# Kernel optimization log

Measured on AMD Instinct MI355X. Metric: run time of the kernel, lower is better.

Reference implementation:

```python
import jax, jax.numpy as jnp
import numpy as np

INPUT_SIZE = 300
HIDDEN = 128
NUM_CLASSES = 2
B, T = 256, 512


def setup_inputs() -> dict:
    key = jax.random.key(0)
    ks = jax.random.split(key, 7)
    s_ih = 1.0 / np.sqrt(HIDDEN)
    x = jax.random.normal(ks[0], (B, T, INPUT_SIZE), dtype=jnp.float32)
    W_ih = jax.random.uniform(ks[1], (HIDDEN, INPUT_SIZE), minval=-s_ih, maxval=s_ih, dtype=jnp.float32)
    W_hh = jax.random.uniform(ks[2], (HIDDEN, HIDDEN), minval=-s_ih, maxval=s_ih, dtype=jnp.float32)
    b_ih = jax.random.uniform(ks[3], (HIDDEN,), minval=-s_ih, maxval=s_ih, dtype=jnp.float32)
    b_hh = jax.random.uniform(ks[4], (HIDDEN,), minval=-s_ih, maxval=s_ih, dtype=jnp.float32)
    fc_w = jax.random.uniform(ks[5], (NUM_CLASSES, HIDDEN), minval=-s_ih, maxval=s_ih, dtype=jnp.float32)
    fc_b = jax.random.uniform(ks[6], (NUM_CLASSES,), minval=-s_ih, maxval=s_ih, dtype=jnp.float32)
    return {"x": x, "W_ih": W_ih, "W_hh": W_hh, "b_ih": b_ih, "b_hh": b_hh, "fc_w": fc_w, "fc_b": fc_b}


def reference(x, W_ih, W_hh, b_ih, b_hh, fc_w, fc_b):
    # Precompute input projections for all timesteps: [B,T,H]
    xp = jnp.einsum('bti,hi->bth', x, W_ih) + b_ih + b_hh
    h0 = jnp.zeros((x.shape[0], HIDDEN), dtype=x.dtype)

    def step(h, xp_t):  # xp_t: [B,H]
        h_new = jnp.tanh(xp_t + h @ W_hh.T)
        return h_new, None

    h_last, _ = jax.lax.scan(step, h0, jnp.swapaxes(xp, 0, 1))  # scan over T
    # Final FC on last hidden state (out[:, -1, :] of the RNN outputs)
    return h_last @ fc_w.T + fc_b
```

## Files before the change

kernel.cpp:

```cpp
#include <hip/hip_runtime.h>
#include <cstdint>
#include <cstddef>

#define KIN 300
#define KPAD 320
#define HIDDEN 128
#define BSZ 256
#define TSZ 512

#define ASTR 332
#define ST1 2176
#define HSTR 136

typedef __attribute__((ext_vector_type(8))) short short8;
typedef __attribute__((ext_vector_type(4))) short s16x4;
typedef __attribute__((ext_vector_type(4))) float f32x4;

__device__ __forceinline__ short f2bf(float f) {
  uint32_t u = __builtin_bit_cast(uint32_t, f);
  u = (u + 0x7FFFu + ((u >> 16) & 1u)) >> 16;
  return (short)u;
}
__device__ __forceinline__ float bf2f(short s) {
  uint32_t u = ((uint32_t)(uint16_t)s) << 16;
  return __builtin_bit_cast(float, u);
}
__device__ __forceinline__ float bflo(uint32_t u) {
  return __builtin_bit_cast(float, u << 16);
}
__device__ __forceinline__ float bfhi(uint32_t u) {
  return __builtin_bit_cast(float, u & 0xFFFF0000u);
}
__device__ __forceinline__ uint32_t pack2bf(float a, float b) {
  uint32_t r;
  asm("v_cvt_pk_bf16_f32 %0, %1, %2" : "=v"(r) : "v"(a), "v"(b));
  return r;
}
__device__ __forceinline__ float tanhf_fast(float v) {
  const float e = __builtin_amdgcn_exp2f(v * 2.88539008177793f);
  return fmaf(-2.0f, __builtin_amdgcn_rcpf(e + 1.0f), 1.0f);
}
__device__ __forceinline__ void barrier_lds() {
  asm volatile("s_waitcnt lgkmcnt(0)\n\ts_barrier" ::: "memory");
}
__device__ __forceinline__ void barrier_all() {
  asm volatile("s_waitcnt vmcnt(0) lgkmcnt(0)\n\ts_barrier" ::: "memory");
}
__device__ __forceinline__ void dma16(const short* g, short* l) {
  __builtin_amdgcn_global_load_lds(
      (const __attribute__((address_space(1))) void*)g,
      (__attribute__((address_space(3))) void*)l, 16, 0, 0);
}

__global__ __launch_bounds__(256) void wcvt_bf16(const float* __restrict__ W,
                                                 short* __restrict__ W16) {
  const int i = blockIdx.x * 256 + threadIdx.x;
  if (i >= HIDDEN * KPAD) return;
  const int n = i / KPAD, k = i % KPAD;
  W16[i] = (k < KIN) ? f2bf(W[n * KIN + k]) : (short)0;
}

__global__ __launch_bounds__(256) void xp_gemm_mfma(
    const float* __restrict__ x, const short* __restrict__ W16,
    const float* __restrict__ b_ih, const float* __restrict__ b_hh,
    short* __restrict__ xp16) {
  __shared__ __align__(16) short As[64 * ASTR];
  const int tid = threadIdx.x;
  const int lane = tid & 63, w = tid >> 6;
  const int q = lane >> 4, c = lane & 15;
  const int bg = blockIdx.x & 15, tc = blockIdx.x >> 4;
  const int b0 = bg * 16, t0 = tc * 4;

#pragma unroll
  for (int i = 0; i < 19; ++i) {
    const int f = tid + 256 * i;
    if (f < 4800) {
      const int rr = f / 75;
      const int k4 = f - rr * 75;
      const int b_in = rr >> 2, t_loc = rr & 3;
      const float4 v = *(const float4*)(
          x + ((size_t)(b0 + b_in) * TSZ + t0 + t_loc) * KIN + k4 * 4);
      uint2 pv;
      pv.x = pack2bf(v.x, v.y);
      pv.y = pack2bf(v.z, v.w);
      *(uint2*)&As[rr * ASTR + k4 * 4] = pv;
    }
  }
  if (tid < 64) {
    const uint2 z = {0u, 0u};
#pragma unroll
    for (int j = 0; j < 5; ++j) *(uint2*)&As[tid * ASTR + 300 + j * 4] = z;
  }
  __syncthreads();

  f32x4 acc[2][4];
#pragma unroll
  for (int ht = 0; ht < 2; ++ht)
#pragma unroll
    for (int rt = 0; rt < 4; ++rt) acc[ht][rt] = (f32x4){0.f, 0.f, 0.f, 0.f};

  const short* wp0 = W16 + (size_t)((2 * w + 0) * 16 + c) * KPAD + q * 8;
  const short* wp1 = W16 + (size_t)((2 * w + 1) * 16 + c) * KPAD + q * 8;
  const short* bqp = &As[c * ASTR + q * 8];
  short8 af[2][2];
  short8 bq[2][4];
  af[0][0] = *(const short8*)(wp0);
  af[0][1] = *(const short8*)(wp1);
#pragma unroll
  for (int rt = 0; rt < 4; ++rt)
    bq[0][rt] = *(const short8*)(bqp + rt * 16 * ASTR);
#pragma unroll
  for (int kc = 0; kc < 10; ++kc) {
    const int cur = kc & 1;
    if (kc < 9) {
      af[cur ^ 1][0] = *(const short8*)(wp0 + (kc + 1) * 32);
      af[cur ^ 1][1] = *(const short8*)(wp1 + (kc + 1) * 32);
#pragma unroll
      for (int rt = 0; rt < 4; ++rt)
        bq[cur ^ 1][rt] = *(const short8*)(bqp + rt * 16 * ASTR + (kc + 1) * 32);
    }
#pragma unroll
    for (int ht = 0; ht < 2; ++ht)
#pragma unroll
      for (int rt = 0; rt < 4; ++rt)
        acc[ht][rt] = __builtin_amdgcn_mfma_f32_16x16x32_bf16(
            af[cur][ht], bq[cur][rt], acc[ht][rt], 0, 0, 0);
  }
  __syncthreads();

  float4 bsum[2];
#pragma unroll
  for (int ht = 0; ht < 2; ++ht) {
    const int h0 = (2 * w + ht) * 16 + q * 4;
    const float4 bi = *(const float4*)(b_ih + h0);
    const float4 bh = *(const float4*)(b_hh + h0);
    bsum[ht] = make_float4(bi.x + bh.x, bi.y + bh.y, bi.z + bh.z, bi.w + bh.w);
  }
#pragma unroll
  for (int ht = 0; ht < 2; ++ht) {
    const int g = (2 * w + ht) * 4 + q;
    const int u = 4 * (g >> 3) + (g & 3);
    const int mt = (g >> 2) & 1;
#pragma unroll
    for (int rt = 0; rt < 4; ++rt) {
      const int b_in = rt * 4 + (c >> 2);
      const int t_loc = c & 3;
      uint2 pv;
      pv.x = pack2bf(acc[ht][rt][0] + bsum[ht].x, acc[ht][rt][1] + bsum[ht].y);
      pv.y = pack2bf(acc[ht][rt][2] + bsum[ht].z, acc[ht][rt][3] + bsum[ht].w);
      *(uint2*)&As[t_loc * ST1 + u * 136 + b_in * 8 + mt * 4] = pv;
    }
  }
  __syncthreads();
#pragma unroll
  for (int i = 0; i < 4; ++i) {
    const int4 vv =
        *(const int4*)&As[i * ST1 + (tid >> 4) * 136 + (tid & 15) * 8];
    *(int4*)(xp16 + ((size_t)(t0 + i) * 16 + bg) * 2048 + tid * 8) = vv;
  }
}

__global__ __launch_bounds__(256, 1) void rnn_scan_dma(
    const short* __restrict__ xp16, const float* __restrict__ Whh,
    const float* __restrict__ fc_w, const float* __restrict__ fc_b,
    float* __restrict__ out) {
  __shared__ __align__(16) short xs[2][8][2048];
  __shared__ __align__(16) short ht[2][16][HSTR];
  const int tid = threadIdx.x;
  const int lane = tid & 63, w = tid >> 6;
  const int q = lane >> 4, c = lane & 15;
  const int bg = blockIdx.x;

  short8 aw[2][4];
#pragma unroll
  for (int mt = 0; mt < 2; ++mt)
#pragma unroll
    for (int kc = 0; kc < 4; ++kc) {
      const float* src =
          Whh + (size_t)(32 * w + 16 * mt + c) * HIDDEN + kc * 32 + q * 8;
      const float4 v0 = *(const float4*)(src);
      const float4 v1 = *(const float4*)(src + 4);
      short8 t;
      t[0] = f2bf(v0.x); t[1] = f2bf(v0.y); t[2] = f2bf(v0.z); t[3] = f2bf(v0.w);
      t[4] = f2bf(v1.x); t[5] = f2bf(v1.y); t[6] = f2bf(v1.z); t[7] = f2bf(v1.w);
      aw[mt][kc] = t;
    }

  {
    uint32_t* z = (uint32_t*)&ht[0][0][0];
    for (int i = tid; i < 2176; i += 256) z[i] = 0;
  }

#define ISSUE_CHUNK(CH, BUF)                                                  \
  {                                                                           \
    _Pragma("unroll") for (int sr = 0; sr < 2; ++sr) {                        \
      const int s = 2 * w + sr;                                               \
      const short* srcb =                                                     \
          xp16 + ((size_t)((CH)*8 + s) * 16 + bg) * 2048 + lane * 8;          \
      _Pragma("unroll") for (int j = 0; j < 4; ++j)                           \
          dma16(srcb + j * 512, &xs[BUF][s][j * 512]);                        \
    }                                                                         \
  }

  ISSUE_CHUNK(0, 0)
  barrier_all();

  const int xsoff = (4 * w + q) * 128 + c * 8;
  const f32x4 zero4 = {0.f, 0.f, 0.f, 0.f};

  for (int cc = 0; cc < 64; ++cc) {
    const int buf = cc & 1;
    if (cc + 1 < 64) ISSUE_CHUNK(cc + 1, buf ^ 1)
    uint4 us[8];
#pragma unroll
    for (int s = 0; s < 8; ++s) us[s] = *(const uint4*)&xs[buf][s][xsoff];
#pragma unroll
    for (int s = 0; s < 8; ++s) {
      const int rb = s & 1;
      const short* bp = &ht[rb][c][q * 8];
      const short8 bh0 = *(const short8*)(bp + 0);
      const short8 bh1 = *(const short8*)(bp + 32);
      const short8 bh2 = *(const short8*)(bp + 64);
      const short8 bh3 = *(const short8*)(bp + 96);
      f32x4 p0 = {bflo(us[s].x), bfhi(us[s].x), bflo(us[s].y), bfhi(us[s].y)};
      f32x4 p1 = {bflo(us[s].z), bfhi(us[s].z), bflo(us[s].w), bfhi(us[s].w)};
      f32x4 r0 = zero4, r1 = zero4;
      p0 = __builtin_amdgcn_mfma_f32_16x16x32_bf16(aw[0][0], bh0, p0, 0, 0, 0);
      r0 = __builtin_amdgcn_mfma_f32_16x16x32_bf16(aw[0][2], bh2, r0, 0, 0, 0);
      p1 = __builtin_amdgcn_mfma_f32_16x16x32_bf16(aw[1][0], bh0, p1, 0, 0, 0);
      r1 = __builtin_amdgcn_mfma_f32_16x16x32_bf16(aw[1][2], bh2, r1, 0, 0, 0);
      p0 = __builtin_amdgcn_mfma_f32_16x16x32_bf16(aw[0][1], bh1, p0, 0, 0, 0);
      r0 = __builtin_amdgcn_mfma_f32_16x16x32_bf16(aw[0][3], bh3, r0, 0, 0, 0);
      p1 = __builtin_amdgcn_mfma_f32_16x16x32_bf16(aw[1][1], bh1, p1, 0, 0, 0);
      r1 = __builtin_amdgcn_mfma_f32_16x16x32_bf16(aw[1][3], bh3, r1, 0, 0, 0);
      const f32x4 s0 = p0 + r0;
      const f32x4 s1 = p1 + r1;
      uint2 w0, w1;
      w0.x = pack2bf(tanhf_fast(s0[0]), tanhf_fast(s0[1]));
      w0.y = pack2bf(tanhf_fast(s0[2]), tanhf_fast(s0[3]));
      w1.x = pack2bf(tanhf_fast(s1[0]), tanhf_fast(s1[1]));
      w1.y = pack2bf(tanhf_fast(s1[2]), tanhf_fast(s1[3]));
      *(uint2*)&ht[rb ^ 1][c][32 * w + 4 * q] = w0;
      *(uint2*)&ht[rb ^ 1][c][32 * w + 16 + 4 * q] = w1;
      barrier_lds();
    }
    barrier_all();
  }
#undef ISSUE_CHUNK

  if (tid < 32) {
    const int bi = tid >> 1, cls = tid & 1;
    float s = fc_b[cls];
    const float* fw = fc_w + cls * HIDDEN;
#pragma unroll 8
    for (int k = 0; k < HIDDEN; k += 4) {
      s = fmaf(bf2f(ht[0][bi][k + 0]), fw[k + 0], s);
      s = fmaf(bf2f(ht[0][bi][k + 1]), fw[k + 1], s);
      s = fmaf(bf2f(ht[0][bi][k + 2]), fw[k + 2], s);
      s = fmaf(bf2f(ht[0][bi][k + 3]), fw[k + 3], s);
    }
    out[(bg * 16 + bi) * 2 + cls] = s;
  }
}

extern "C" void kernel_launch(void* const* d_in, const int* in_sizes, int n_in,
                              void* d_out, int out_size, void* d_ws, size_t ws_size,
                              hipStream_t stream) {
  const float* x    = (const float*)d_in[0];
  const float* W_ih = (const float*)d_in[1];
  const float* W_hh = (const float*)d_in[2];
  const float* b_ih = (const float*)d_in[3];
  const float* b_hh = (const float*)d_in[4];
  const float* fc_w = (const float*)d_in[5];
  const float* fc_b = (const float*)d_in[6];
  short* xp16 = (short*)d_ws;
  short* W16  = (short*)((char*)d_ws + (33u << 20));
  float* out  = (float*)d_out;

  wcvt_bf16<<<(HIDDEN * KPAD + 255) / 256, 256, 0, stream>>>(W_ih, W16);
  xp_gemm_mfma<<<16 * (TSZ / 4), 256, 0, stream>>>(x, W16, b_ih, b_hh, xp16);
  rnn_scan_dma<<<16, 256, 0, stream>>>(xp16, W_hh, fc_w, fc_b, out);
}
```

Measured before the change: 455.5 us.

## Run two independent batch recurrences per 512-thread block with swizzled hidden state

The scan kernel now uses 8 blocks of 512 threads, each running two independent 16-row batch recurrences (one per group of four waves) that share the block barriers, instead of 16 blocks of 256 threads. Hidden-state LDS storage moves to an XOR-swizzled layout without padding, meant to avoid bank conflicts. Chunks now hold 4 timesteps over 128 iterations rather than 8 over 64. The aim is to interleave two recurrence chains on one CU to hide MFMA and tanh latency, but it uses half as many CUs and each barrier now waits on both chains and more waves.

```diff
diff --git a/kernel.cpp b/kernel.cpp
--- a/kernel.cpp
+++ b/kernel.cpp
@@ -10,7 +10,6 @@
 
 #define ASTR 332
 #define ST1 2176
-#define HSTR 136
 
 typedef __attribute__((ext_vector_type(8))) short short8;
 typedef __attribute__((ext_vector_type(4))) short s16x4;
@@ -160,16 +159,18 @@
   }
 }
 
-__global__ __launch_bounds__(256, 1) void rnn_scan_dma(
+__global__ __launch_bounds__(512, 1) void rnn_scan_dma(
     const short* __restrict__ xp16, const float* __restrict__ Whh,
     const float* __restrict__ fc_w, const float* __restrict__ fc_b,
     float* __restrict__ out) {
-  __shared__ __align__(16) short xs[2][8][2048];
-  __shared__ __align__(16) short ht[2][16][HSTR];
+  __shared__ __align__(16) short xs[2][4][2][2048];
+  __shared__ __align__(16) short hts[8192];
   const int tid = threadIdx.x;
   const int lane = tid & 63, w = tid >> 6;
   const int q = lane >> 4, c = lane & 15;
+  const int rec = w >> 2, rw = w & 3;
   const int bg = blockIdx.x;
+  const int c7 = c & 7;
 
   short8 aw[2][4];
 #pragma unroll
@@ -177,7 +178,7 @@
 #pragma unroll
     for (int kc = 0; kc < 4; ++kc) {
       const float* src =
-          Whh + (size_t)(32 * w + 16 * mt + c) * HIDDEN + kc * 32 + q * 8;
+          Whh + (size_t)(32 * rw + 16 * mt + c) * HIDDEN + kc * 32 + q * 8;
       const float4 v0 = *(const float4*)(src);
       const float4 v1 = *(const float4*)(src + 4);
       short8 t;
@@ -186,45 +187,54 @@
       aw[mt][kc] = t;
     }
 
-  {
-    uint32_t* z = (uint32_t*)&ht[0][0][0];
-    for (int i = tid; i < 2176; i += 256) z[i] = 0;
-  }
+  for (int i = tid; i < 4096; i += 512) ((uint32_t*)hts)[i] = 0;
 
 #define ISSUE_CHUNK(CH, BUF)                                                  \
   {                                                                           \
-    _Pragma("unroll") for (int sr = 0; sr < 2; ++sr) {                        \
-      const int s = 2 * w + sr;                                               \
-      const short* srcb =                                                     \
-          xp16 + ((size_t)((CH)*8 + s) * 16 + bg) * 2048 + lane * 8;          \
-      _Pragma("unroll") for (int j = 0; j < 4; ++j)                           \
-          dma16(srcb + j * 512, &xs[BUF][s][j * 512]);                        \
-    }                                                                         \
+    const short* srcb =                                                       \
+        xp16 + ((size_t)((CH)*4 + rw) * 16 + (2 * bg + rec)) * 2048 +         \
+        lane * 8;                                                             \
+    _Pragma("unroll") for (int j = 0; j < 4; ++j)                             \
+        dma16(srcb + j * 512, &xs[BUF][rw][rec][j * 512]);                    \
   }
 
   ISSUE_CHUNK(0, 0)
   barrier_all();
 
-  const int xsoff = (4 * w + q) * 128 + c * 8;
-  const f32x4 zero4 = {0.f, 0.f, 0.f, 0.f};
-
-  for (int cc = 0; cc < 64; ++cc) {
+  const int rbase0 = ((rec * 2 + 0) * 16 + c) * 128;
+  const int rbase1 = rbase0 + 16 * 128;
+  const short* rp0[4];
+  const short* rp1[4];
+#pragma unroll
+  for (int kc = 0; kc < 4; ++kc) {
+    const int off = ((4 * kc + q) ^ c7) * 8;
+    rp0[kc] = hts + rbase0 + off;
+    rp1[kc] = hts + rbase1 + off;
+  }
+  const int wo0 = ((4 * rw + (q >> 1)) ^ c7) * 8 + 4 * (q & 1);
+  const int wo1 = ((4 * rw + 2 + (q >> 1)) ^ c7) * 8 + 4 * (q & 1);
+  short* const wb0 = hts + rbase0;
+  short* const wb1 = hts + rbase1;
+
+  const int xsoff = (4 * rw + q) * 128 + c * 8;
+
+  for (int cc = 0; cc < 128; ++cc) {
     const int buf = cc & 1;
-    if (cc + 1 < 64) ISSUE_CHUNK(cc + 1, buf ^ 1)
-    uint4 us[8];
-#pragma unroll
-    for (int s = 0; s < 8; ++s) us[s] = *(const uint4*)&xs[buf][s][xsoff];
-#pragma unroll
-    for (int s = 0; s < 8; ++s) {
+    if (cc + 1 < 128) ISSUE_CHUNK(cc + 1, buf ^ 1)
+    uint4 us[4];
+#pragma unroll
+    for (int s = 0; s < 4; ++s) us[s] = *(const uint4*)&xs[buf][s][rec][xsoff];
+#pragma unroll
+    for (int s = 0; s < 4; ++s) {
       const int rb = s & 1;
-      const short* bp = &ht[rb][c][q * 8];
-      const short8 bh0 = *(const short8*)(bp + 0);
-      const short8 bh1 = *(const short8*)(bp + 32);
-      const short8 bh2 = *(const short8*)(bp + 64);
-      const short8 bh3 = *(const short8*)(bp + 96);
+      const short8 bh0 = *(const short8*)(rb ? rp1[0] : rp0[0]);
+      const short8 bh1 = *(const short8*)(rb ? rp1[1] : rp0[1]);
+      const short8 bh2 = *(const short8*)(rb ? rp1[2] : rp0[2]);
+      const short8 bh3 = *(const short8*)(rb ? rp1[3] : rp0[3]);
       f32x4 p0 = {bflo(us[s].x), bfhi(us[s].x), bflo(us[s].y), bfhi(us[s].y)};
       f32x4 p1 = {bflo(us[s].z), bfhi(us[s].z), bflo(us[s].w), bfhi(us[s].w)};
-      f32x4 r0 = zero4, r1 = zero4;
+      f32x4 r0 = {0.f, 0.f, 0.f, 0.f};
+      f32x4 r1 = {0.f, 0.f, 0.f, 0.f};
       p0 = __builtin_amdgcn_mfma_f32_16x16x32_bf16(aw[0][0], bh0, p0, 0, 0, 0);
       r0 = __builtin_amdgcn_mfma_f32_16x16x32_bf16(aw[0][2], bh2, r0, 0, 0, 0);
       p1 = __builtin_amdgcn_mfma_f32_16x16x32_bf16(aw[1][0], bh0, p1, 0, 0, 0);
@@ -240,26 +250,30 @@
       w0.y = pack2bf(tanhf_fast(s0[2]), tanhf_fast(s0[3]));
       w1.x = pack2bf(tanhf_fast(s1[0]), tanhf_fast(s1[1]));
       w1.y = pack2bf(tanhf_fast(s1[2]), tanhf_fast(s1[3]));
-      *(uint2*)&ht[rb ^ 1][c][32 * w + 4 * q] = w0;
-      *(uint2*)&ht[rb ^ 1][c][32 * w + 16 + 4 * q] = w1;
+      short* const wb = rb ? wb0 : wb1;
+      *(uint2*)(wb + wo0) = w0;
+      *(uint2*)(wb + wo1) = w1;
       barrier_lds();
     }
     barrier_all();
   }
 #undef ISSUE_CHUNK
 
-  if (tid < 32) {
-    const int bi = tid >> 1, cls = tid & 1;
-    float s = fc_b[cls];
+  if (tid < 64) {
+    const int bi2 = tid >> 1;
+    const int r_ = bi2 >> 4, bi = bi2 & 15, cls = tid & 1;
+    float sacc = fc_b[cls];
     const float* fw = fc_w + cls * HIDDEN;
-#pragma unroll 8
-    for (int k = 0; k < HIDDEN; k += 4) {
-      s = fmaf(bf2f(ht[0][bi][k + 0]), fw[k + 0], s);
-      s = fmaf(bf2f(ht[0][bi][k + 1]), fw[k + 1], s);
-      s = fmaf(bf2f(ht[0][bi][k + 2]), fw[k + 2], s);
-      s = fmaf(bf2f(ht[0][bi][k + 3]), fw[k + 3], s);
-    }
-    out[(bg * 16 + bi) * 2 + cls] = s;
+    const short* hb = hts + ((r_ * 2 + 0) * 16 + bi) * 128;
+    const int b7 = bi & 7;
+#pragma unroll 4
+    for (int g = 0; g < 16; ++g) {
+      const short* gp = hb + (g ^ b7) * 8;
+#pragma unroll
+      for (int j = 0; j < 8; ++j)
+        sacc = fmaf(bf2f(gp[j]), fw[g * 8 + j], sacc);
+    }
+    out[(bg * 32 + r_ * 16 + bi) * 2 + cls] = sacc;
   }
 }
 
@@ -279,5 +293,5 @@
 
   wcvt_bf16<<<(HIDDEN * KPAD + 255) / 256, 256, 0, stream>>>(W_ih, W16);
   xp_gemm_mfma<<<16 * (TSZ / 4), 256, 0, stream>>>(x, W16, b_ih, b_hh, xp16);
-  rnn_scan_dma<<<16, 256, 0, stream>>>(xp16, W_hh, fc_w, fc_b, out);
-}
+  rnn_scan_dma<<<8, 512, 0, stream>>>(xp16, W_hh, fc_w, fc_b, out);
+}
```

Result: slower. 534.6 us (+17.4%).
